# Optimization experiments

Measured on AMD Instinct MI355X. Metric: run time of the kernel, lower is better.

The kernel has to match this reference:

```python
import jax, jax.numpy as jnp
import numpy as np
from jax.scipy.special import ndtr

EPS1 = 1e-6
WEIGHT_DECAY = 1e-5  # FLAGS.weight_decay


def setup_inputs() -> dict:
    key = jax.random.key(0)
    ks = jax.random.split(key, 12)
    B, F, C, Z, S = 512, 512, 500, 64, 100  # batch, features, classes (r_dim), z_dim, n_sample
    lim = np.sqrt(6.0 / (C + Z))
    def glorot(k, shape):
        fan_in, fan_out = shape
        s = np.sqrt(2.0 / (fan_in + fan_out))
        return jax.random.normal(k, shape, jnp.float32) * s
    return {
        "input_X": jax.random.normal(ks[0], (B, F), jnp.float32),
        "input_Y": (jax.random.uniform(ks[1], (B, C)) < 0.1).astype(jnp.float32),  # multi-label targets
        "noise": jax.random.normal(ks[2], (S, B, Z), jnp.float32),
        "W1": glorot(ks[3], (F, 128)), "b1": jnp.zeros((128,), jnp.float32),
        "W2": glorot(ks[4], (128, 256)), "b2": jnp.zeros((256,), jnp.float32),
        "W3": glorot(ks[5], (256, 256)), "b3": jnp.zeros((256,), jnp.float32),
        "Wmu": glorot(ks[6], (256, C)), "bmu": jnp.zeros((C,), jnp.float32),
        "r_sqrt_sigma": jax.random.uniform(ks[7], (C, Z), jnp.float32, -lim, lim),
    }


def reference(input_X, input_Y, noise, W1, b1, W2, b2, W3, b3, Wmu, bmu, r_sqrt_sigma):
    # MLP trunk
    h = jax.nn.relu(input_X @ W1 + b1)
    h = jax.nn.relu(h @ W2 + b2)
    feature = jax.nn.relu(h @ W3 + b3)

    # low-rank covariance: sigma = R R^T, covariance = sigma + I
    cov_diag = jnp.sum(r_sqrt_sigma * r_sqrt_sigma, axis=1) + 1.0  # [C]

    normalized_mu = feature @ Wmu + bmu            # [B, C]
    r_mu = normalized_mu * jnp.sqrt(cov_diag)      # [B, C]

    # MC samples of latent r: [S, B, C]
    sample_r = jnp.einsum('sbz,cz->sbc', noise, r_sqrt_sigma) + r_mu

    E = ndtr(sample_r) * (1.0 - EPS1) + EPS1 * 0.5  # probit CDF, clamped
    # logprob = sum_c [ Y*log(E) + (1-Y)*log(1-E) ]  (== -sum sample_nll)
    logprob = jnp.sum(jnp.log(E) * input_Y + jnp.log1p(-E) * (1.0 - input_Y), axis=2)  # [S, B]
    maxlogprob = jnp.max(logprob, axis=0)                       # [B]
    Eprob = jnp.mean(jnp.exp(logprob - maxlogprob), axis=0)     # [B]
    nll_loss = jnp.mean(-jnp.log(Eprob) - maxlogprob)

    # marginal (independent) probit approximated by scaled sigmoid
    indiv_prob = jax.nn.sigmoid(normalized_mu * 1.70169) * (1.0 - EPS1) + 0.5 * EPS1
    cross_entropy = jnp.log(indiv_prob) * input_Y + jnp.log1p(-indiv_prob) * (1.0 - input_Y)
    marginal_loss = -jnp.mean(jnp.sum(cross_entropy, axis=1))

    l2_loss = WEIGHT_DECAY * (jnp.sum(W1 * W1) + jnp.sum(W2 * W2)
                              + jnp.sum(W3 * W3) + jnp.sum(Wmu * Wmu))
    total_loss = l2_loss + nll_loss
    return indiv_prob, nll_loss, marginal_loss, l2_loss, total_loss
```

## Files before the change

### kernel.cpp

```cpp
#include <hip/hip_runtime.h>
#include <cstddef>

#define EPS1f 1e-6f
#define WDf   1e-5f

constexpr int Bsz = 512, Fsz = 512, Csz = 500, Zsz = 64, Ssz = 100;

typedef short bf16x8 __attribute__((ext_vector_type(8)));
typedef float f32x4 __attribute__((ext_vector_type(4)));

__device__ inline short f2bf(float f) {
  union { float f; unsigned u; } v; v.f = f;
  unsigned r = (v.u + 0x7fffu + ((v.u >> 16) & 1u)) >> 16;
  return (short)r;
}

__device__ inline float log_probit(float t) {
  const float u = t * -0.70710678118654752f;
  const float au = fabsf(u);
  const float s = 1.f / fmaf(0.3275911f, au, 1.f);
  float p = fmaf(1.061405429f, s, -1.453152027f);
  p = fmaf(p, s, 1.421413741f);
  p = fmaf(p, s, -0.284496736f);
  p = fmaf(p, s, 0.254829592f);
  p = p * s;
  const float e = __expf(-au * au);
  const float f = p * e;
  const float erfc_u = (u < 0.f) ? (2.f - f) : f;
  const float E = fmaf(0.5f * erfc_u, 1.f - EPS1f, 0.5f * EPS1f);
  return __logf(E);
}

__device__ inline float block_reduce_sum(float v, float* red) {
  #pragma unroll
  for (int off = 32; off > 0; off >>= 1) v += __shfl_down(v, off, 64);
  const int lane = threadIdx.x & 63, wid = threadIdx.x >> 6;
  if (lane == 0) red[wid] = v;
  __syncthreads();
  float r = 0.f;
  if (threadIdx.x == 0) {
    const int nw = blockDim.x >> 6;
    for (int i = 0; i < nw; ++i) r += red[i];
  }
  __syncthreads();
  return r;
}

__device__ __forceinline__ void gemm32_body(
    const float* __restrict__ A, const float* __restrict__ W,
    const float* __restrict__ bias, float* __restrict__ out,
    int M, int N, int K, int bn0, int bm0, float* As_, float* Ws_, bool relu) {
  const int tid = threadIdx.x;
  const int bn = bn0 * 32, bm = bm0 * 32;
  const int sm = tid >> 3, sk4 = (tid & 7) * 4;
  const int sk = tid >> 3, sn4 = (tid & 7) * 4;
  const int tn = tid & 15, tm = tid >> 4;
  #define AS_(b, k, m) As_[(b) * 1152 + (k) * 36 + (m)]
  #define WS_(b, k, n) Ws_[(b) * 1152 + (k) * 36 + (n)]

  auto loadW = [&](int kt, float4& wv) {
    const float* wrow = W + (size_t)(kt + sk) * N;
    const int nn = bn + sn4;
    if (nn + 3 < N) wv = *reinterpret_cast<const float4*>(wrow + nn);
    else {
      wv.x = (nn + 0 < N) ? wrow[nn + 0] : 0.f;
      wv.y = (nn + 1 < N) ? wrow[nn + 1] : 0.f;
      wv.z = (nn + 2 < N) ? wrow[nn + 2] : 0.f;
      wv.w = (nn + 3 < N) ? wrow[nn + 3] : 0.f;
    }
  };
  {
    float4 av = *reinterpret_cast<const float4*>(A + (size_t)(bm + sm) * K + sk4);
    float4 wv; loadW(0, wv);
    AS_(0, sk4 + 0, sm) = av.x; AS_(0, sk4 + 1, sm) = av.y;
    AS_(0, sk4 + 2, sm) = av.z; AS_(0, sk4 + 3, sm) = av.w;
    *reinterpret_cast<float4*>(&WS_(0, sk, sn4)) = wv;
  }
  __syncthreads();
  float acc[2][2] = {};
  int pb = 0;
  for (int kt = 0; kt < K; kt += 32) {
    const bool more = (kt + 32) < K;
    float4 av2, wv2;
    if (more) {
      av2 = *reinterpret_cast<const float4*>(A + (size_t)(bm + sm) * K + kt + 32 + sk4);
      loadW(kt + 32, wv2);
    }
    #pragma unroll
    for (int k = 0; k < 32; ++k) {
      const float2 a = *reinterpret_cast<const float2*>(&AS_(pb, k, tm * 2));
      const float2 w = *reinterpret_cast<const float2*>(&WS_(pb, k, tn * 2));
      acc[0][0] = fmaf(a.x, w.x, acc[0][0]);
      acc[0][1] = fmaf(a.x, w.y, acc[0][1]);
      acc[1][0] = fmaf(a.y, w.x, acc[1][0]);
      acc[1][1] = fmaf(a.y, w.y, acc[1][1]);
    }
    if (more) {
      const int nb = pb ^ 1;
      AS_(nb, sk4 + 0, sm) = av2.x; AS_(nb, sk4 + 1, sm) = av2.y;
      AS_(nb, sk4 + 2, sm) = av2.z; AS_(nb, sk4 + 3, sm) = av2.w;
      *reinterpret_cast<float4*>(&WS_(nb, sk, sn4)) = wv2;
      __syncthreads();
      pb = nb;
    }
  }
  #pragma unroll
  for (int j = 0; j < 2; ++j) {
    const int n = bn + tn * 2 + j;
    if (n >= N) continue;
    const float bv = bias[n];
    #pragma unroll
    for (int i = 0; i < 2; ++i) {
      const int m = bm + tm * 2 + i;
      float v = acc[i][j] + bv;
      if (relu) v = fmaxf(v, 0.f);
      out[(size_t)m * N + n] = v;
    }
  }
  #undef AS_
  #undef WS_
}

__global__ __launch_bounds__(256) void prep_kernel(
    const float* __restrict__ noise, short* __restrict__ nfB,
    const float* __restrict__ R, short* __restrict__ Rb, float* __restrict__ sqrtcov,
    const float* __restrict__ X, const float* __restrict__ W1,
    const float* __restrict__ b1, float* __restrict__ h1,
    const float* __restrict__ W2, const float* __restrict__ W3,
    const float* __restrict__ Wmu, float* __restrict__ l2_part) {
  __shared__ float smem[2304 * 2];
  const int blk = blockIdx.x;
  const int tid = threadIdx.x;
  if (blk < 800) {
    const int g = blk * 256 + tid;
    const int s = g >> 11;
    const int r = g & 2047;
    const int bt = r >> 6;
    const int ln = r & 63;
    const int cl = ln & 15, grp = ln >> 4;
    const float* src = noise + ((size_t)(s * 512 + bt * 16 + cl) * 64 + grp * 8);
    const float4 a = *reinterpret_cast<const float4*>(src);
    const float4 b = *reinterpret_cast<const float4*>(src + 4);
    const float4 c = *reinterpret_cast<const float4*>(src + 32);
    const float4 d = *reinterpret_cast<const float4*>(src + 36);
    bf16x8* dst = reinterpret_cast<bf16x8*>(nfB);
    const int u = (s * 32 + bt) * 128 + ln;
    dst[u]      = bf16x8{ f2bf(a.x), f2bf(a.y), f2bf(a.z), f2bf(a.w),
                          f2bf(b.x), f2bf(b.y), f2bf(b.z), f2bf(b.w) };
    dst[u + 64] = bf16x8{ f2bf(c.x), f2bf(c.y), f2bf(c.z), f2bf(c.w),
                          f2bf(d.x), f2bf(d.y), f2bf(d.z), f2bf(d.w) };
  } else if (blk < 808) {
    const int idx = (blk - 800) * 256 + tid;
    const int c = idx >> 2;
    const int zq = (idx & 3) * 16;
    const bool cv = c < Csz;
    const float* src = R + (size_t)c * Zsz + zq;
    float4 r0, r1, r2, r3;
    if (cv) {
      r0 = *reinterpret_cast<const float4*>(src);
      r1 = *reinterpret_cast<const float4*>(src + 4);
      r2 = *reinterpret_cast<const float4*>(src + 8);
      r3 = *reinterpret_cast<const float4*>(src + 12);
    } else {
      r0 = r1 = r2 = r3 = make_float4(0.f, 0.f, 0.f, 0.f);
    }
    float ss = 0.f;
    ss = fmaf(r0.x, r0.x, ss); ss = fmaf(r0.y, r0.y, ss);
    ss = fmaf(r0.z, r0.z, ss); ss = fmaf(r0.w, r0.w, ss);
    ss = fmaf(r1.x, r1.x, ss); ss = fmaf(r1.y, r1.y, ss);
    ss = fmaf(r1.z, r1.z, ss); ss = fmaf(r1.w, r1.w, ss);
    ss = fmaf(r2.x, r2.x, ss); ss = fmaf(r2.y, r2.y, ss);
    ss = fmaf(r2.z, r2.z, ss); ss = fmaf(r2.w, r2.w, ss);
    ss = fmaf(r3.x, r3.x, ss); ss = fmaf(r3.y, r3.y, ss);
    ss = fmaf(r3.z, r3.z, ss); ss = fmaf(r3.w, r3.w, ss);
    short* dst = Rb + (size_t)c * Zsz + zq;
    *reinterpret_cast<bf16x8*>(dst) =
        bf16x8{ f2bf(r0.x), f2bf(r0.y), f2bf(r0.z), f2bf(r0.w),
                f2bf(r1.x), f2bf(r1.y), f2bf(r1.z), f2bf(r1.w) };
    *reinterpret_cast<bf16x8*>(dst + 8) =
        bf16x8{ f2bf(r2.x), f2bf(r2.y), f2bf(r2.z), f2bf(r2.w),
                f2bf(r3.x), f2bf(r3.y), f2bf(r3.z), f2bf(r3.w) };
    ss += __shfl_xor(ss, 1, 64);
    ss += __shfl_xor(ss, 2, 64);
    if ((idx & 3) == 0 && cv) sqrtcov[c] = sqrtf(1.f + ss);
  } else if (blk < 872) {
    const int bid = blk - 808;
    const int gid = bid * 256 + tid;
    const int stride = 64 * 256;
    float s = 0.f;
    for (int i = gid; i < 65536; i += stride) { float v = W1[i]; s = fmaf(v, v, s); }
    for (int i = gid; i < 32768; i += stride) { float v = W2[i]; s = fmaf(v, v, s); }
    for (int i = gid; i < 65536; i += stride) { float v = W3[i]; s = fmaf(v, v, s); }
    for (int i = gid; i < 128000; i += stride) { float v = Wmu[i]; s = fmaf(v, v, s); }
    const float tot = block_reduce_sum(s, smem);
    if (tid == 0) l2_part[bid] = tot;
  } else {
    const int idx = blk - 872;
    gemm32_body(X, W1, b1, h1, 512, 128, 512, idx & 3, idx >> 2,
                smem, smem + 2304, true);
  }
}

template <bool RELU>
__global__ __launch_bounds__(256) void gemm32(
    const float* __restrict__ A, const float* __restrict__ W,
    const float* __restrict__ bias, float* __restrict__ out,
    int M, int N, int K) {
  __shared__ float smem[2304 * 2];
  gemm32_body(A, W, bias, out, M, N, K, blockIdx.x, blockIdx.y,
              smem, smem + 2304, RELU);
}

__global__ __launch_bounds__(256) void gemm32_mu(
    const float* __restrict__ A, const float* __restrict__ W,
    const float* __restrict__ bias, const float* __restrict__ Y,
    const float* __restrict__ sqrtcov,
    float* __restrict__ out_prob, float* __restrict__ rmuB, float* __restrict__ yB,
    float* __restrict__ ce_part, int M, int N, int K) {
  __shared__ float As[2][32][36];
  __shared__ float Ws[2][32][36];
  const int tid = threadIdx.x;
  const int bn = blockIdx.x * 32, bm = blockIdx.y * 32;
  const int sm = tid >> 3, sk4 = (tid & 7) * 4;
  const int sk = tid >> 3, sn4 = (tid & 7) * 4;
  const int tn = tid & 15, tm = tid >> 4;

  auto loadW = [&](int kt, float4& wv) {
    const float* wrow = W + (size_t)(kt + sk) * N;
    const int nn = bn + sn4;
    if (nn + 3 < N) wv = *reinterpret_cast<const float4*>(wrow + nn);
    else {
      wv.x = (nn + 0 < N) ? wrow[nn + 0] : 0.f;
      wv.y = (nn + 1 < N) ? wrow[nn + 1] : 0.f;
      wv.z = (nn + 2 < N) ? wrow[nn + 2] : 0.f;
      wv.w = (nn + 3 < N) ? wrow[nn + 3] : 0.f;
    }
  };
  {
    float4 av = *reinterpret_cast<const float4*>(A + (size_t)(bm + sm) * K + sk4);
    float4 wv; loadW(0, wv);
    As[0][sk4 + 0][sm] = av.x; As[0][sk4 + 1][sm] = av.y;
    As[0][sk4 + 2][sm] = av.z; As[0][sk4 + 3][sm] = av.w;
    *reinterpret_cast<float4*>(&Ws[0][sk][sn4]) = wv;
  }
  __syncthreads();
  float acc[2][2] = {};
  int pb = 0;
  for (int kt = 0; kt < K; kt += 32) {
    const bool more = (kt + 32) < K;
    float4 av2, wv2;
    if (more) {
      av2 = *reinterpret_cast<const float4*>(A + (size_t)(bm + sm) * K + kt + 32 + sk4);
      loadW(kt + 32, wv2);
    }
    #pragma unroll
    for (int k = 0; k < 32; ++k) {
      const float2 a = *reinterpret_cast<const float2*>(&As[pb][k][tm * 2]);
      const float2 w = *reinterpret_cast<const float2*>(&Ws[pb][k][tn * 2]);
      acc[0][0] = fmaf(a.x, w.x, acc[0][0]);
      acc[0][1] = fmaf(a.x, w.y, acc[0][1]);
      acc[1][0] = fmaf(a.y, w.x, acc[1][0]);
      acc[1][1] = fmaf(a.y, w.y, acc[1][1]);
    }
    if (more) {
      const int nb = pb ^ 1;
      As[nb][sk4 + 0][sm] = av2.x; As[nb][sk4 + 1][sm] = av2.y;
      As[nb][sk4 + 2][sm] = av2.z; As[nb][sk4 + 3][sm] = av2.w;
      *reinterpret_cast<float4*>(&Ws[nb][sk][sn4]) = wv2;
      __syncthreads();
      pb = nb;
    }
  }
  float ce2[2] = {0.f, 0.f};
  #pragma unroll
  for (int i = 0; i < 2; ++i) {
    const int m = bm + tm * 2 + i;
    #pragma unroll
    for (int j = 0; j < 2; ++j) {
      const int n = bn + tn * 2 + j;
      if (n < N) {
        const float v = acc[i][j] + bias[n];
        const float sp = 1.f / (1.f + __expf(-1.70169f * v));
        const float p = fmaf(sp, 1.f - EPS1f, 0.5f * EPS1f);
        const float q = fmaf(1.f - sp, 1.f - EPS1f, 0.5f * EPS1f);
        const float y = Y[(size_t)m * N + n];
        out_prob[(size_t)m * N + n] = p;
        ce2[i] += __logf((y > 0.5f) ? p : q);
        rmuB[(size_t)m * 512 + n] = v * sqrtcov[n];
        yB[(size_t)m * 512 + n] = y;
      }
    }
  }
  #pragma unroll
  for (int off = 1; off < 16; off <<= 1) {
    ce2[0] += __shfl_xor(ce2[0], off, 64);
    ce2[1] += __shfl_xor(ce2[1], off, 64);
  }
  if (tn == 0) {
    const int m0 = bm + tm * 2;
    ce_part[(size_t)blockIdx.x * Bsz + m0] = ce2[0];
    ce_part[(size_t)blockIdx.x * Bsz + m0 + 1] = ce2[1];
  }
}

__global__ __launch_bounds__(256, 8) void logprob_s(
    const short* __restrict__ nfB, const short* __restrict__ Rb,
    const float* __restrict__ rmuB, const float* __restrict__ yB,
    float* __restrict__ lp_part) {
  const int blk = blockIdx.x;
  const int bt = blk & 31;
  const int ctg = (blk >> 5) & 7;
  const int sg = blk >> 8;
  const int wid = threadIdx.x >> 6;
  const int lane = threadIdx.x & 63;
  const int cl = lane & 15, grp = lane >> 4;
  const int ct = ctg * 4 + wid;
  const int c0 = ct * 16, b0 = bt * 16;

  const bf16x8 Rf0 = *reinterpret_cast<const bf16x8*>(Rb + (size_t)(c0 + cl) * 64 + grp * 8);
  const bf16x8 Rf1 = *reinterpret_cast<const bf16x8*>(Rb + (size_t)(c0 + cl) * 64 + 32 + grp * 8);
  const int cb = c0 + grp * 4;
  const float4 rmu4 = *reinterpret_cast<const float4*>(rmuB + (size_t)(b0 + cl) * 512 + cb);
  const float4 y4   = *reinterpret_cast<const float4*>(yB + (size_t)(b0 + cl) * 512 + cb);
  const float sg0 = fmaf(2.f, y4.x, -1.f), sg1 = fmaf(2.f, y4.y, -1.f);
  const float sg2 = fmaf(2.f, y4.z, -1.f), sg3 = fmaf(2.f, y4.w, -1.f);
  const bool v0 = cb + 0 < Csz, v1 = cb + 1 < Csz, v2 = cb + 2 < Csz, v3 = cb + 3 < Csz;

  const bf16x8* nf = reinterpret_cast<const bf16x8*>(nfB);
  const int sbase = sg * 10;
  int base = (sbase * 32 + bt) * 128 + lane;
  bf16x8 c0f = nf[base], c1f = nf[base + 64];

  for (int i = 0; i < 10; ++i) {
    const int nbase = base + 4096;
    bf16x8 p0, p1;
    if (i < 9) { p0 = nf[nbase]; p1 = nf[nbase + 64]; }
    f32x4 acc = {0.f, 0.f, 0.f, 0.f};
    acc = __builtin_amdgcn_mfma_f32_16x16x32_bf16(Rf0, c0f, acc, 0, 0, 0);
    acc = __builtin_amdgcn_mfma_f32_16x16x32_bf16(Rf1, c1f, acc, 0, 0, 0);
    float lpl = 0.f;
    lpl += v0 ? log_probit((acc[0] + rmu4.x) * sg0) : 0.f;
    lpl += v1 ? log_probit((acc[1] + rmu4.y) * sg1) : 0.f;
    lpl += v2 ? log_probit((acc[2] + rmu4.z) * sg2) : 0.f;
    lpl += v3 ? log_probit((acc[3] + rmu4.w) * sg3) : 0.f;
    lpl += __shfl_xor(lpl, 16, 64);
    lpl += __shfl_xor(lpl, 32, 64);
    if (lane < 16) {
      const int s = sbase + i;
      lp_part[(size_t)(s * 32 + ct) * 512 + b0 + lane] = lpl;
    }
    c0f = p0; c1f = p1; base = nbase;
  }
}

__global__ __launch_bounds__(256) void ctsum(const float* __restrict__ lp_part,
                                             float* __restrict__ lp_sum) {
  const int i = blockIdx.x * 256 + threadIdx.x;
  const int s = i >> 9, b = i & 511;
  const float* p = lp_part + (size_t)s * 16384 + b;
  float a0 = 0.f, a1 = 0.f, a2 = 0.f, a3 = 0.f;
  #pragma unroll
  for (int ct = 0; ct < 32; ct += 4) {
    a0 += p[(ct + 0) * 512];
    a1 += p[(ct + 1) * 512];
    a2 += p[(ct + 2) * 512];
    a3 += p[(ct + 3) * 512];
  }
  lp_sum[i] = (a0 + a1) + (a2 + a3);
}

__global__ __launch_bounds__(256) void nll_kernel(const float* __restrict__ lp_sum,
                                                  float* __restrict__ nll_b) {
  __shared__ float sm[4][64], sse[4][64];
  const int bl = threadIdx.x & 63;
  const int sc = threadIdx.x >> 6;
  const int b = blockIdx.x * 64 + bl;
  float m = -3.0e38f, se = 0.f;
  for (int s = sc * 25; s < sc * 25 + 25; ++s) {
    const float v = lp_sum[(size_t)s * Bsz + b];
    const float mn = fmaxf(m, v);
    se = se * __expf(m - mn) + __expf(v - mn);
    m = mn;
  }
  sm[sc][bl] = m; sse[sc][bl] = se;
  __syncthreads();
  if (sc == 0) {
    float M = sm[0][bl];
    #pragma unroll
    for (int i = 1; i < 4; ++i) M = fmaxf(M, sm[i][bl]);
    float SE = 0.f;
    #pragma unroll
    for (int i = 0; i < 4; ++i) SE += sse[i][bl] * __expf(sm[i][bl] - M);
    nll_b[b] = -__logf(SE * (1.f / (float)Ssz)) - M;
  }
}

__global__ __launch_bounds__(256) void finals_kernel(
    const float* __restrict__ nll_b, const float* __restrict__ ce_part,
    const float* __restrict__ l2_part, int nparts, float* __restrict__ out4) {
  __shared__ float red[4];
  const int t = threadIdx.x;
  const float snll = block_reduce_sum(nll_b[t] + nll_b[t + 256], red);
  float ce = 0.f;
  #pragma unroll
  for (int i = 0; i < 32; ++i) ce += ce_part[i * 256 + t];
  const float sce = block_reduce_sum(ce, red);
  const float sl2 = block_reduce_sum((t < nparts) ? l2_part[t] : 0.f, red);
  if (t == 0) {
    const float nll = snll / (float)Bsz;
    const float marg = -sce / (float)Bsz;
    const float l2v = WDf * sl2;
    out4[0] = nll;
    out4[1] = marg;
    out4[2] = l2v;
    out4[3] = l2v + nll;
  }
}

extern "C" void kernel_launch(void* const* d_in, const int* in_sizes, int n_in,
                              void* d_out, int out_size, void* d_ws, size_t ws_size,
                              hipStream_t stream) {
  const float* X = (const float*)d_in[0];
  const float* Y = (const float*)d_in[1];
  const float* noise = (const float*)d_in[2];
  const float* W1 = (const float*)d_in[3];
  const float* b1 = (const float*)d_in[4];
  const float* W2 = (const float*)d_in[5];
  const float* b2 = (const float*)d_in[6];
  const float* W3 = (const float*)d_in[7];
  const float* b3 = (const float*)d_in[8];
  const float* Wmu = (const float*)d_in[9];
  const float* bmu = (const float*)d_in[10];
  const float* rss = (const float*)d_in[11];

  float* ws = (float*)d_ws;
  float* lp_part = ws;
  float* h1 = ws;
  float* h2 = h1 + 65536;
  float* feat = h2 + 131072;
  float* B0 = ws + 1638400;
  float* sqrtcov = B0;
  float* rmuB = sqrtcov + 512;
  float* yB = rmuB + 262144;
  float* ce_part = yB + 262144;
  float* nll_b = ce_part + 8192;
  float* l2_part = nll_b + 512;
  float* lp_sum = l2_part + 128;
  short* Rb = (short*)(lp_sum + 51200);
  short* nfB = (short*)(lp_sum + 51200 + 16384);

  float* out_prob = (float*)d_out;
  float* out4 = out_prob + (size_t)Bsz * Csz;

  prep_kernel<<<dim3(936), 256, 0, stream>>>(noise, nfB, rss, Rb, sqrtcov,
                                             X, W1, b1, h1, W2, W3, Wmu, l2_part);

  gemm32<true><<<dim3(8, 16), 256, 0, stream>>>(h1, W2, b2, h2, 512, 256, 128);
  gemm32<true><<<dim3(8, 16), 256, 0, stream>>>(h2, W3, b3, feat, 512, 256, 256);
  gemm32_mu<<<dim3(16, 16), 256, 0, stream>>>(feat, Wmu, bmu, Y, sqrtcov,
                                              out_prob, rmuB, yB, ce_part, 512, 500, 256);

  logprob_s<<<dim3(2560), 256, 0, stream>>>(nfB, Rb, rmuB, yB, lp_part);
  ctsum<<<dim3(200), 256, 0, stream>>>(lp_part, lp_sum);
  nll_kernel<<<dim3(8), 256, 0, stream>>>(lp_sum, nll_b);

  finals_kernel<<<dim3(1), 256, 0, stream>>>(nll_b, ce_part, l2_part, 64, out4);
}
```

Baseline: 86.75 us.

## Fuse class-tile sum into NLL kernel and process two samples per iteration

The logprob kernel now handles two samples per loop iteration, issuing interleaved MFMAs and prefetching two samples ahead to raise instruction-level parallelism. The separate ctsum kernel is removed. The NLL kernel now launches one block per batch element, and each block sums the 32 class-tile partials per sample before a shared-memory logsumexp tree reduction. This drops one kernel launch and the lp_sum round trip. In exchange, the NLL kernel's reads of lp_part are strided and leave many threads idle.

```diff
diff --git a/kernel.cpp b/kernel.cpp
--- a/kernel.cpp
+++ b/kernel.cpp
@@ -4,7 +4,7 @@
 #define EPS1f 1e-6f
 #define WDf   1e-5f
 
-constexpr int Bsz = 512, Fsz = 512, Csz = 500, Zsz = 64, Ssz = 100;
+constexpr int Bsz = 512, Csz = 500, Zsz = 64, Ssz = 100;
 
 typedef short bf16x8 __attribute__((ext_vector_type(8)));
 typedef float f32x4 __attribute__((ext_vector_type(4)));
@@ -57,7 +57,6 @@
   const int tn = tid & 15, tm = tid >> 4;
   #define AS_(b, k, m) As_[(b) * 1152 + (k) * 36 + (m)]
   #define WS_(b, k, n) Ws_[(b) * 1152 + (k) * 36 + (n)]
-
   auto loadW = [&](int kt, float4& wv) {
     const float* wrow = W + (size_t)(kt + sk) * N;
     const int nn = bn + sn4;
@@ -322,77 +321,85 @@
   const int cb = c0 + grp * 4;
   const float4 rmu4 = *reinterpret_cast<const float4*>(rmuB + (size_t)(b0 + cl) * 512 + cb);
   const float4 y4   = *reinterpret_cast<const float4*>(yB + (size_t)(b0 + cl) * 512 + cb);
-  const float sg0 = fmaf(2.f, y4.x, -1.f), sg1 = fmaf(2.f, y4.y, -1.f);
-  const float sg2 = fmaf(2.f, y4.z, -1.f), sg3 = fmaf(2.f, y4.w, -1.f);
+  const float sn0 = fmaf(2.f, y4.x, -1.f), sn1 = fmaf(2.f, y4.y, -1.f);
+  const float sn2 = fmaf(2.f, y4.z, -1.f), sn3 = fmaf(2.f, y4.w, -1.f);
   const bool v0 = cb + 0 < Csz, v1 = cb + 1 < Csz, v2 = cb + 2 < Csz, v3 = cb + 3 < Csz;
 
   const bf16x8* nf = reinterpret_cast<const bf16x8*>(nfB);
   const int sbase = sg * 10;
   int base = (sbase * 32 + bt) * 128 + lane;
-  bf16x8 c0f = nf[base], c1f = nf[base + 64];
-
-  for (int i = 0; i < 10; ++i) {
-    const int nbase = base + 4096;
-    bf16x8 p0, p1;
-    if (i < 9) { p0 = nf[nbase]; p1 = nf[nbase + 64]; }
-    f32x4 acc = {0.f, 0.f, 0.f, 0.f};
-    acc = __builtin_amdgcn_mfma_f32_16x16x32_bf16(Rf0, c0f, acc, 0, 0, 0);
-    acc = __builtin_amdgcn_mfma_f32_16x16x32_bf16(Rf1, c1f, acc, 0, 0, 0);
-    float lpl = 0.f;
-    lpl += v0 ? log_probit((acc[0] + rmu4.x) * sg0) : 0.f;
-    lpl += v1 ? log_probit((acc[1] + rmu4.y) * sg1) : 0.f;
-    lpl += v2 ? log_probit((acc[2] + rmu4.z) * sg2) : 0.f;
-    lpl += v3 ? log_probit((acc[3] + rmu4.w) * sg3) : 0.f;
-    lpl += __shfl_xor(lpl, 16, 64);
-    lpl += __shfl_xor(lpl, 32, 64);
+
+  bf16x8 fa0 = nf[base],        fa1 = nf[base + 64];
+  bf16x8 fb0 = nf[base + 4096], fb1 = nf[base + 4096 + 64];
+
+  #pragma unroll 1
+  for (int i = 0; i < 10; i += 2) {
+    bf16x8 na0, na1, nb0, nb1;
+    if (i < 8) {
+      na0 = nf[base + 8192];  na1 = nf[base + 8192 + 64];
+      nb0 = nf[base + 12288]; nb1 = nf[base + 12288 + 64];
+    }
+    f32x4 accA = {0.f, 0.f, 0.f, 0.f};
+    f32x4 accB = {0.f, 0.f, 0.f, 0.f};
+    accA = __builtin_amdgcn_mfma_f32_16x16x32_bf16(Rf0, fa0, accA, 0, 0, 0);
+    accB = __builtin_amdgcn_mfma_f32_16x16x32_bf16(Rf0, fb0, accB, 0, 0, 0);
+    accA = __builtin_amdgcn_mfma_f32_16x16x32_bf16(Rf1, fa1, accA, 0, 0, 0);
+    accB = __builtin_amdgcn_mfma_f32_16x16x32_bf16(Rf1, fb1, accB, 0, 0, 0);
+    float lpA = 0.f, lpB = 0.f;
+    lpA += v0 ? log_probit((accA[0] + rmu4.x) * sn0) : 0.f;
+    lpB += v0 ? log_probit((accB[0] + rmu4.x) * sn0) : 0.f;
+    lpA += v1 ? log_probit((accA[1] + rmu4.y) * sn1) : 0.f;
+    lpB += v1 ? log_probit((accB[1] + rmu4.y) * sn1) : 0.f;
+    lpA += v2 ? log_probit((accA[2] + rmu4.z) * sn2) : 0.f;
+    lpB += v2 ? log_probit((accB[2] + rmu4.z) * sn2) : 0.f;
+    lpA += v3 ? log_probit((accA[3] + rmu4.w) * sn3) : 0.f;
+    lpB += v3 ? log_probit((accB[3] + rmu4.w) * sn3) : 0.f;
+    lpA += __shfl_xor(lpA, 16, 64);
+    lpA += __shfl_xor(lpA, 32, 64);
+    lpB += __shfl_xor(lpB, 16, 64);
+    lpB += __shfl_xor(lpB, 32, 64);
     if (lane < 16) {
       const int s = sbase + i;
-      lp_part[(size_t)(s * 32 + ct) * 512 + b0 + lane] = lpl;
-    }
-    c0f = p0; c1f = p1; base = nbase;
-  }
-}
-
-__global__ __launch_bounds__(256) void ctsum(const float* __restrict__ lp_part,
-                                             float* __restrict__ lp_sum) {
-  const int i = blockIdx.x * 256 + threadIdx.x;
-  const int s = i >> 9, b = i & 511;
-  const float* p = lp_part + (size_t)s * 16384 + b;
-  float a0 = 0.f, a1 = 0.f, a2 = 0.f, a3 = 0.f;
-  #pragma unroll
-  for (int ct = 0; ct < 32; ct += 4) {
-    a0 += p[(ct + 0) * 512];
-    a1 += p[(ct + 1) * 512];
-    a2 += p[(ct + 2) * 512];
-    a3 += p[(ct + 3) * 512];
-  }
-  lp_sum[i] = (a0 + a1) + (a2 + a3);
-}
-
-__global__ __launch_bounds__(256) void nll_kernel(const float* __restrict__ lp_sum,
+      lp_part[(size_t)(s * 32 + ct) * 512 + b0 + lane] = lpA;
+      lp_part[(size_t)((s + 1) * 32 + ct) * 512 + b0 + lane] = lpB;
+    }
+    base += 8192;
+    fa0 = na0; fa1 = na1; fb0 = nb0; fb1 = nb1;
+  }
+}
+
+__global__ __launch_bounds__(256) void nll_kernel(const float* __restrict__ lp_part,
                                                   float* __restrict__ nll_b) {
-  __shared__ float sm[4][64], sse[4][64];
-  const int bl = threadIdx.x & 63;
-  const int sc = threadIdx.x >> 6;
-  const int b = blockIdx.x * 64 + bl;
+  __shared__ float sm[256], ss[256];
+  const int b = blockIdx.x;
+  const int tid = threadIdx.x;
   float m = -3.0e38f, se = 0.f;
-  for (int s = sc * 25; s < sc * 25 + 25; ++s) {
-    const float v = lp_sum[(size_t)s * Bsz + b];
-    const float mn = fmaxf(m, v);
-    se = se * __expf(m - mn) + __expf(v - mn);
-    m = mn;
-  }
-  sm[sc][bl] = m; sse[sc][bl] = se;
+  if (tid < Ssz) {
+    const float* p = lp_part + (size_t)tid * 16384 + b;
+    float a0 = 0.f, a1 = 0.f, a2 = 0.f, a3 = 0.f;
+    #pragma unroll
+    for (int ct = 0; ct < 32; ct += 4) {
+      a0 += p[(ct + 0) * 512];
+      a1 += p[(ct + 1) * 512];
+      a2 += p[(ct + 2) * 512];
+      a3 += p[(ct + 3) * 512];
+    }
+    m = (a0 + a1) + (a2 + a3);
+    se = 1.f;
+  }
+  sm[tid] = m; ss[tid] = se;
   __syncthreads();
-  if (sc == 0) {
-    float M = sm[0][bl];
-    #pragma unroll
-    for (int i = 1; i < 4; ++i) M = fmaxf(M, sm[i][bl]);
-    float SE = 0.f;
-    #pragma unroll
-    for (int i = 0; i < 4; ++i) SE += sse[i][bl] * __expf(sm[i][bl] - M);
-    nll_b[b] = -__logf(SE * (1.f / (float)Ssz)) - M;
-  }
+  #pragma unroll
+  for (int off = 128; off > 0; off >>= 1) {
+    if (tid < off) {
+      const float m1 = sm[tid], m2 = sm[tid + off];
+      const float M = fmaxf(m1, m2);
+      ss[tid] = ss[tid] * __expf(m1 - M) + ss[tid + off] * __expf(m2 - M);
+      sm[tid] = M;
+    }
+    __syncthreads();
+  }
+  if (tid == 0) nll_b[b] = -__logf(ss[0] * (1.f / (float)Ssz)) - sm[0];
 }
 
 __global__ __launch_bounds__(256) void finals_kernel(
@@ -445,9 +452,8 @@
   float* ce_part = yB + 262144;
   float* nll_b = ce_part + 8192;
   float* l2_part = nll_b + 512;
-  float* lp_sum = l2_part + 128;
-  short* Rb = (short*)(lp_sum + 51200);
-  short* nfB = (short*)(lp_sum + 51200 + 16384);
+  short* Rb = (short*)(l2_part + 128);
+  short* nfB = (short*)(l2_part + 128 + 16384);
 
   float* out_prob = (float*)d_out;
   float* out4 = out_prob + (size_t)Bsz * Csz;
@@ -461,8 +467,7 @@
                                               out_prob, rmuB, yB, ce_part, 512, 500, 256);
 
   logprob_s<<<dim3(2560), 256, 0, stream>>>(nfB, Rb, rmuB, yB, lp_part);
-  ctsum<<<dim3(200), 256, 0, stream>>>(lp_part, lp_sum);
-  nll_kernel<<<dim3(8), 256, 0, stream>>>(lp_sum, nll_b);
+  nll_kernel<<<dim3(512), 256, 0, stream>>>(lp_part, nll_b);
 
   finals_kernel<<<dim3(1), 256, 0, stream>>>(nll_b, ce_part, l2_part, 64, out4);
 }
```

Measured after the change: 93.16 us. 7.4% more time.

## Restructure logprob kernel to loop over class tiles and drop ctsum pass

Applied to the files above, without the earlier changes.

The logprob kernel now gives each wave a fixed noise fragment (one sample, one batch tile) and loops over 16 class tiles, accumulating the log-likelihood in registers. This replaces the old scheme that wrote a partial per class tile and then needed a separate ctsum reduction kernel. R is pre-packed into MFMA fragment order, and rmu and the sign of Y are stored in a fragment-tiled layout so each iteration reads them with one contiguous float4. The cost is fewer blocks with more serial work per wave, plus an extra prep branch and a lower occupancy hint.

```diff
diff --git a/kernel.cpp b/kernel.cpp
--- a/kernel.cpp
+++ b/kernel.cpp
@@ -4,7 +4,7 @@
 #define EPS1f 1e-6f
 #define WDf   1e-5f
 
-constexpr int Bsz = 512, Fsz = 512, Csz = 500, Zsz = 64, Ssz = 100;
+constexpr int Bsz = 512, Csz = 500, Zsz = 64, Ssz = 100;
 
 typedef short bf16x8 __attribute__((ext_vector_type(8)));
 typedef float f32x4 __attribute__((ext_vector_type(4)));
@@ -57,7 +57,6 @@
   const int tn = tid & 15, tm = tid >> 4;
   #define AS_(b, k, m) As_[(b) * 1152 + (k) * 36 + (m)]
   #define WS_(b, k, n) Ws_[(b) * 1152 + (k) * 36 + (n)]
-
   auto loadW = [&](int kt, float4& wv) {
     const float* wrow = W + (size_t)(kt + sk) * N;
     const int nn = bn + sn4;
@@ -123,7 +122,7 @@
 
 __global__ __launch_bounds__(256) void prep_kernel(
     const float* __restrict__ noise, short* __restrict__ nfB,
-    const float* __restrict__ R, short* __restrict__ Rb, float* __restrict__ sqrtcov,
+    const float* __restrict__ R, short* __restrict__ RbF, float* __restrict__ sqrtcov,
     const float* __restrict__ X, const float* __restrict__ W1,
     const float* __restrict__ b1, float* __restrict__ h1,
     const float* __restrict__ W2, const float* __restrict__ W3,
@@ -155,36 +154,36 @@
     const int zq = (idx & 3) * 16;
     const bool cv = c < Csz;
     const float* src = R + (size_t)c * Zsz + zq;
-    float4 r0, r1, r2, r3;
+    float ss = 0.f;
     if (cv) {
-      r0 = *reinterpret_cast<const float4*>(src);
-      r1 = *reinterpret_cast<const float4*>(src + 4);
-      r2 = *reinterpret_cast<const float4*>(src + 8);
-      r3 = *reinterpret_cast<const float4*>(src + 12);
-    } else {
-      r0 = r1 = r2 = r3 = make_float4(0.f, 0.f, 0.f, 0.f);
-    }
-    float ss = 0.f;
-    ss = fmaf(r0.x, r0.x, ss); ss = fmaf(r0.y, r0.y, ss);
-    ss = fmaf(r0.z, r0.z, ss); ss = fmaf(r0.w, r0.w, ss);
-    ss = fmaf(r1.x, r1.x, ss); ss = fmaf(r1.y, r1.y, ss);
-    ss = fmaf(r1.z, r1.z, ss); ss = fmaf(r1.w, r1.w, ss);
-    ss = fmaf(r2.x, r2.x, ss); ss = fmaf(r2.y, r2.y, ss);
-    ss = fmaf(r2.z, r2.z, ss); ss = fmaf(r2.w, r2.w, ss);
-    ss = fmaf(r3.x, r3.x, ss); ss = fmaf(r3.y, r3.y, ss);
-    ss = fmaf(r3.z, r3.z, ss); ss = fmaf(r3.w, r3.w, ss);
-    short* dst = Rb + (size_t)c * Zsz + zq;
-    *reinterpret_cast<bf16x8*>(dst) =
-        bf16x8{ f2bf(r0.x), f2bf(r0.y), f2bf(r0.z), f2bf(r0.w),
-                f2bf(r1.x), f2bf(r1.y), f2bf(r1.z), f2bf(r1.w) };
-    *reinterpret_cast<bf16x8*>(dst + 8) =
-        bf16x8{ f2bf(r2.x), f2bf(r2.y), f2bf(r2.z), f2bf(r2.w),
-                f2bf(r3.x), f2bf(r3.y), f2bf(r3.z), f2bf(r3.w) };
+      #pragma unroll
+      for (int q = 0; q < 4; ++q) {
+        const float4 r4 = *reinterpret_cast<const float4*>(src + q * 4);
+        ss = fmaf(r4.x, r4.x, ss); ss = fmaf(r4.y, r4.y, ss);
+        ss = fmaf(r4.z, r4.z, ss); ss = fmaf(r4.w, r4.w, ss);
+      }
+    }
     ss += __shfl_xor(ss, 1, 64);
     ss += __shfl_xor(ss, 2, 64);
     if ((idx & 3) == 0 && cv) sqrtcov[c] = sqrtf(1.f + ss);
-  } else if (blk < 872) {
-    const int bid = blk - 808;
+  } else if (blk < 824) {
+    const int e = (blk - 808) * 256 + tid;
+    const int ct = e >> 7;
+    const int f = (e >> 6) & 1;
+    const int lane = e & 63;
+    const int cl = lane & 15, grp = lane >> 4;
+    const int c = ct * 16 + cl;
+    bf16x8 out = {0, 0, 0, 0, 0, 0, 0, 0};
+    if (c < Csz) {
+      const float* src = R + (size_t)c * Zsz + f * 32 + grp * 8;
+      const float4 a = *reinterpret_cast<const float4*>(src);
+      const float4 b = *reinterpret_cast<const float4*>(src + 4);
+      out = bf16x8{ f2bf(a.x), f2bf(a.y), f2bf(a.z), f2bf(a.w),
+                    f2bf(b.x), f2bf(b.y), f2bf(b.z), f2bf(b.w) };
+    }
+    reinterpret_cast<bf16x8*>(RbF)[e] = out;
+  } else if (blk < 888) {
+    const int bid = blk - 824;
     const int gid = bid * 256 + tid;
     const int stride = 64 * 256;
     float s = 0.f;
@@ -195,7 +194,7 @@
     const float tot = block_reduce_sum(s, smem);
     if (tid == 0) l2_part[bid] = tot;
   } else {
-    const int idx = blk - 872;
+    const int idx = blk - 888;
     gemm32_body(X, W1, b1, h1, 512, 128, 512, idx & 3, idx >> 2,
                 smem, smem + 2304, true);
   }
@@ -215,7 +214,7 @@
     const float* __restrict__ A, const float* __restrict__ W,
     const float* __restrict__ bias, const float* __restrict__ Y,
     const float* __restrict__ sqrtcov,
-    float* __restrict__ out_prob, float* __restrict__ rmuB, float* __restrict__ yB,
+    float* __restrict__ out_prob, float* __restrict__ rmuP, float* __restrict__ snP,
     float* __restrict__ ce_part, int M, int N, int K) {
   __shared__ float As[2][32][36];
   __shared__ float Ws[2][32][36];
@@ -286,8 +285,10 @@
         const float y = Y[(size_t)m * N + n];
         out_prob[(size_t)m * N + n] = p;
         ce2[i] += __logf((y > 0.5f) ? p : q);
-        rmuB[(size_t)m * 512 + n] = v * sqrtcov[n];
-        yB[(size_t)m * 512 + n] = y;
+        const int idx = (((n >> 4) * 32 + (m >> 4)) << 8)
+                      + ((((n >> 2) & 3) * 16 + (m & 15)) << 2) + (n & 3);
+        rmuP[idx] = v * sqrtcov[n];
+        snP[idx] = (y > 0.5f) ? 1.f : -1.f;
       }
     }
   }
@@ -303,73 +304,49 @@
   }
 }
 
-__global__ __launch_bounds__(256, 8) void logprob_s(
-    const short* __restrict__ nfB, const short* __restrict__ Rb,
-    const float* __restrict__ rmuB, const float* __restrict__ yB,
-    float* __restrict__ lp_part) {
+__global__ __launch_bounds__(256, 6) void logprob_s2(
+    const short* __restrict__ nfB, const short* __restrict__ RbF,
+    const float* __restrict__ rmuP, const float* __restrict__ snP,
+    float* __restrict__ lp2) {
   const int blk = blockIdx.x;
-  const int bt = blk & 31;
-  const int ctg = (blk >> 5) & 7;
-  const int sg = blk >> 8;
+  const int btg = blk & 15;
+  const int s = blk >> 4;
   const int wid = threadIdx.x >> 6;
   const int lane = threadIdx.x & 63;
-  const int cl = lane & 15, grp = lane >> 4;
-  const int ct = ctg * 4 + wid;
-  const int c0 = ct * 16, b0 = bt * 16;
-
-  const bf16x8 Rf0 = *reinterpret_cast<const bf16x8*>(Rb + (size_t)(c0 + cl) * 64 + grp * 8);
-  const bf16x8 Rf1 = *reinterpret_cast<const bf16x8*>(Rb + (size_t)(c0 + cl) * 64 + 32 + grp * 8);
-  const int cb = c0 + grp * 4;
-  const float4 rmu4 = *reinterpret_cast<const float4*>(rmuB + (size_t)(b0 + cl) * 512 + cb);
-  const float4 y4   = *reinterpret_cast<const float4*>(yB + (size_t)(b0 + cl) * 512 + cb);
-  const float sg0 = fmaf(2.f, y4.x, -1.f), sg1 = fmaf(2.f, y4.y, -1.f);
-  const float sg2 = fmaf(2.f, y4.z, -1.f), sg3 = fmaf(2.f, y4.w, -1.f);
-  const bool v0 = cb + 0 < Csz, v1 = cb + 1 < Csz, v2 = cb + 2 < Csz, v3 = cb + 3 < Csz;
+  const int bt = btg * 2 + (wid & 1);
+  const int ch = wid >> 1;
+  const int grp = lane >> 4;
 
   const bf16x8* nf = reinterpret_cast<const bf16x8*>(nfB);
-  const int sbase = sg * 10;
-  int base = (sbase * 32 + bt) * 128 + lane;
-  bf16x8 c0f = nf[base], c1f = nf[base + 64];
-
-  for (int i = 0; i < 10; ++i) {
-    const int nbase = base + 4096;
-    bf16x8 p0, p1;
-    if (i < 9) { p0 = nf[nbase]; p1 = nf[nbase + 64]; }
+  const int nbase = (s * 32 + bt) * 128 + lane;
+  const bf16x8 n0 = nf[nbase];
+  const bf16x8 n1 = nf[nbase + 64];
+  const bf16x8* rf = reinterpret_cast<const bf16x8*>(RbF);
+
+  float lpl = 0.f;
+  #pragma unroll 2
+  for (int t = 0; t < 16; ++t) {
+    const int ct = ch * 16 + t;
+    const bf16x8 Rf0 = rf[(ct * 2 + 0) * 64 + lane];
+    const bf16x8 Rf1 = rf[(ct * 2 + 1) * 64 + lane];
     f32x4 acc = {0.f, 0.f, 0.f, 0.f};
-    acc = __builtin_amdgcn_mfma_f32_16x16x32_bf16(Rf0, c0f, acc, 0, 0, 0);
-    acc = __builtin_amdgcn_mfma_f32_16x16x32_bf16(Rf1, c1f, acc, 0, 0, 0);
-    float lpl = 0.f;
-    lpl += v0 ? log_probit((acc[0] + rmu4.x) * sg0) : 0.f;
-    lpl += v1 ? log_probit((acc[1] + rmu4.y) * sg1) : 0.f;
-    lpl += v2 ? log_probit((acc[2] + rmu4.z) * sg2) : 0.f;
-    lpl += v3 ? log_probit((acc[3] + rmu4.w) * sg3) : 0.f;
-    lpl += __shfl_xor(lpl, 16, 64);
-    lpl += __shfl_xor(lpl, 32, 64);
-    if (lane < 16) {
-      const int s = sbase + i;
-      lp_part[(size_t)(s * 32 + ct) * 512 + b0 + lane] = lpl;
-    }
-    c0f = p0; c1f = p1; base = nbase;
-  }
-}
-
-__global__ __launch_bounds__(256) void ctsum(const float* __restrict__ lp_part,
-                                             float* __restrict__ lp_sum) {
-  const int i = blockIdx.x * 256 + threadIdx.x;
-  const int s = i >> 9, b = i & 511;
-  const float* p = lp_part + (size_t)s * 16384 + b;
-  float a0 = 0.f, a1 = 0.f, a2 = 0.f, a3 = 0.f;
-  #pragma unroll
-  for (int ct = 0; ct < 32; ct += 4) {
-    a0 += p[(ct + 0) * 512];
-    a1 += p[(ct + 1) * 512];
-    a2 += p[(ct + 2) * 512];
-    a3 += p[(ct + 3) * 512];
-  }
-  lp_sum[i] = (a0 + a1) + (a2 + a3);
-}
-
-__global__ __launch_bounds__(256) void nll_kernel(const float* __restrict__ lp_sum,
+    acc = __builtin_amdgcn_mfma_f32_16x16x32_bf16(Rf0, n0, acc, 0, 0, 0);
+    acc = __builtin_amdgcn_mfma_f32_16x16x32_bf16(Rf1, n1, acc, 0, 0, 0);
+    const int fb = (ct * 32 + bt) * 256 + lane * 4;
+    const float4 rmu4 = *reinterpret_cast<const float4*>(rmuP + fb);
+    const float4 sn4  = *reinterpret_cast<const float4*>(snP + fb);
+    const int cb = ct * 16 + grp * 4;
+    lpl += (cb + 0 < Csz) ? log_probit((acc[0] + rmu4.x) * sn4.x) : 0.f;
+    lpl += (cb + 1 < Csz) ? log_probit((acc[1] + rmu4.y) * sn4.y) : 0.f;
+    lpl += (cb + 2 < Csz) ? log_probit((acc[2] + rmu4.z) * sn4.z) : 0.f;
+    lpl += (cb + 3 < Csz) ? log_probit((acc[3] + rmu4.w) * sn4.w) : 0.f;
+  }
+  lpl += __shfl_xor(lpl, 16, 64);
+  lpl += __shfl_xor(lpl, 32, 64);
+  if (lane < 16) lp2[(size_t)(ch * Ssz + s) * 512 + bt * 16 + lane] = lpl;
+}
+
+__global__ __launch_bounds__(256) void nll_kernel(const float* __restrict__ lp2,
                                                   float* __restrict__ nll_b) {
   __shared__ float sm[4][64], sse[4][64];
   const int bl = threadIdx.x & 63;
@@ -377,7 +354,7 @@
   const int b = blockIdx.x * 64 + bl;
   float m = -3.0e38f, se = 0.f;
   for (int s = sc * 25; s < sc * 25 + 25; ++s) {
-    const float v = lp_sum[(size_t)s * Bsz + b];
+    const float v = lp2[(size_t)s * 512 + b] + lp2[(size_t)(Ssz + s) * 512 + b];
     const float mn = fmaxf(m, v);
     se = se * __expf(m - mn) + __expf(v - mn);
     m = mn;
@@ -434,35 +411,33 @@
   const float* rss = (const float*)d_in[11];
 
   float* ws = (float*)d_ws;
-  float* lp_part = ws;
   float* h1 = ws;
   float* h2 = h1 + 65536;
   float* feat = h2 + 131072;
-  float* B0 = ws + 1638400;
+  float* B0 = ws + 327680;
   float* sqrtcov = B0;
-  float* rmuB = sqrtcov + 512;
-  float* yB = rmuB + 262144;
-  float* ce_part = yB + 262144;
+  float* rmuP = sqrtcov + 512;
+  float* snP = rmuP + 262144;
+  float* ce_part = snP + 262144;
   float* nll_b = ce_part + 8192;
   float* l2_part = nll_b + 512;
-  float* lp_sum = l2_part + 128;
-  short* Rb = (short*)(lp_sum + 51200);
-  short* nfB = (short*)(lp_sum + 51200 + 16384);
+  float* lp2 = l2_part + 128;
+  short* RbF = (short*)(lp2 + 102400);
+  short* nfB = RbF + 32768;
 
   float* out_prob = (float*)d_out;
   float* out4 = out_prob + (size_t)Bsz * Csz;
 
-  prep_kernel<<<dim3(936), 256, 0, stream>>>(noise, nfB, rss, Rb, sqrtcov,
+  prep_kernel<<<dim3(952), 256, 0, stream>>>(noise, nfB, rss, RbF, sqrtcov,
                                              X, W1, b1, h1, W2, W3, Wmu, l2_part);
 
   gemm32<true><<<dim3(8, 16), 256, 0, stream>>>(h1, W2, b2, h2, 512, 256, 128);
   gemm32<true><<<dim3(8, 16), 256, 0, stream>>>(h2, W3, b3, feat, 512, 256, 256);
   gemm32_mu<<<dim3(16, 16), 256, 0, stream>>>(feat, Wmu, bmu, Y, sqrtcov,
-                                              out_prob, rmuB, yB, ce_part, 512, 500, 256);
-
-  logprob_s<<<dim3(2560), 256, 0, stream>>>(nfB, Rb, rmuB, yB, lp_part);
-  ctsum<<<dim3(200), 256, 0, stream>>>(lp_part, lp_sum);
-  nll_kernel<<<dim3(8), 256, 0, stream>>>(lp_sum, nll_b);
+                                              out_prob, rmuP, snP, ce_part, 512, 500, 256);
+
+  logprob_s2<<<dim3(1600), 256, 0, stream>>>(nfB, RbF, rmuP, snP, lp2);
+  nll_kernel<<<dim3(8), 256, 0, stream>>>(lp2, nll_b);
 
   finals_kernel<<<dim3(1), 256, 0, stream>>>(nll_b, ce_part, l2_part, 64, out4);
 }
```

After: 87.51 us. No clear change (+0.9%).
